# Performance work log

Hardware: AMD Instinct MI355X
Metric: run time of the kernel (lower is better)

## Reference

```python
import jax, jax.numpy as jnp
import numpy as np

MAX_V = 100000.0
CLAMP = 8.0


def setup_inputs() -> dict:
    key = jax.random.key(0)
    point = jax.random.normal(key, (8, 4096, 3), dtype=jnp.float32)
    return {"point": point}


def reference(point):
    # point: [B, N, D]
    p = point.astype(jnp.float32)
    N = p.shape[1]
    # ||a-b|| via ||a||^2 + ||b||^2 - 2 a.b (avoids the [B,N,N,D] diff tensor
    # the torch original materializes; same math up to fp rounding)
    sq = jnp.sum(p * p, axis=-1)                       # [B, N]
    d2 = sq[:, :, None] + sq[:, None, :] - 2.0 * jnp.einsum('bnd,bmd->bnm', p, p)
    dist = jnp.sqrt(jnp.maximum(d2, 0.0))              # [B, N, N]
    dist = dist + jnp.eye(N, dtype=jnp.float32) * MAX_V  # bigeye: kill diagonal
    min_dist = jnp.min(dist, axis=2)                   # [B, N] nearest-neighbor dist
    c = jnp.max(min_dist, axis=1)                      # [B] farthest-point distance
    return jnp.maximum(c, CLAMP)
```

## Files before the change

kernel.cpp:

```cpp
#include <hip/hip_runtime.h>
#include <math.h>

#define NB       8
#define NPTS     4096
#define CLAMP    8.0f
#define CLAMP2   64.0f
#define BIG      3.0e38f

#define THREADS  1024
#define QPT      4
#define SAMPLES  64
#define CHUNK    8


__global__ __launch_bounds__(THREADS)
void mmpd_batch(const float* __restrict__ pts, float* __restrict__ out) {
    __shared__ float sp[SAMPLES * 3];
    __shared__ float allp[NPTS * 3];
    __shared__ unsigned int wflag[16];
    __shared__ unsigned int sflag;
    __shared__ float wmaxs[16];

    const int tid  = threadIdx.x;
    const int b    = blockIdx.x;
    const int lane = tid & 63;
    const int wid  = tid >> 6;
    const float* __restrict__ base = pts + (size_t)b * (NPTS * 3);

    if (tid < (SAMPLES * 3 / 4))
        ((float4*)sp)[tid] = ((const float4*)base)[tid];
    __syncthreads();

    const int q0 = tid * QPT;
    const float4 f0 = ((const float4*)base)[tid * 3 + 0];
    const float4 f1 = ((const float4*)base)[tid * 3 + 1];
    const float4 f2 = ((const float4*)base)[tid * 3 + 2];
    const float qx[QPT] = {f0.x, f0.w, f1.z, f2.y};
    const float qy[QPT] = {f0.y, f1.x, f1.w, f2.z};
    const float qz[QPT] = {f0.z, f1.y, f2.x, f2.w};

    float mn[QPT] = {BIG, BIG, BIG, BIG};

    for (int i = 0; i < SAMPLES; i += CHUNK) {
        #pragma unroll
        for (int k = 0; k < CHUNK; ++k) {
            const int s = i + k;
            const float px = sp[3 * s + 0];
            const float py = sp[3 * s + 1];
            const float pz = sp[3 * s + 2];
            #pragma unroll
            for (int j = 0; j < QPT; ++j) {
                const float dx = qx[j] - px;
                const float dy = qy[j] - py;
                const float dz = qz[j] - pz;
                const float d2 = dx * dx + dy * dy + dz * dz;
                mn[j] = fminf(mn[j], (s == q0 + j) ? BIG : d2);
            }
        }
        const bool over = (mn[0] > CLAMP2) | (mn[1] > CLAMP2) |
                          (mn[2] > CLAMP2) | (mn[3] > CLAMP2);
        if (__ballot(over) == 0ull) break;
    }

    {
        const bool over = (mn[0] > CLAMP2) | (mn[1] > CLAMP2) |
                          (mn[2] > CLAMP2) | (mn[3] > CLAMP2);
        const unsigned long long bal = __ballot(over);
        if (lane == 0) wflag[wid] = (bal != 0ull) ? 1u : 0u;
    }
    __syncthreads();
    if (tid == 0) {
        unsigned int f = 0;
        #pragma unroll
        for (int w = 0; w < 16; ++w) f |= wflag[w];
        sflag = f;
    }
    __syncthreads();

    if (sflag == 0u) {
        if (tid == 0) out[b] = CLAMP;
        return;
    }

    #pragma unroll
    for (int k = 0; k < 3; ++k)
        ((float4*)allp)[tid + k * THREADS] = ((const float4*)base)[tid + k * THREADS];
    __syncthreads();

    float ex[QPT] = {BIG, BIG, BIG, BIG};
    for (int m = 0; m < NPTS; ++m) {
        const float px = allp[3 * m + 0];
        const float py = allp[3 * m + 1];
        const float pz = allp[3 * m + 2];
        #pragma unroll
        for (int j = 0; j < QPT; ++j) {
            const float dx = qx[j] - px;
            const float dy = qy[j] - py;
            const float dz = qz[j] - pz;
            const float d2 = dx * dx + dy * dy + dz * dz;
            ex[j] = fminf(ex[j], (m == q0 + j) ? BIG : d2);
        }
    }

    float v = fmaxf(fmaxf(ex[0], ex[1]), fmaxf(ex[2], ex[3]));
    #pragma unroll
    for (int off = 32; off >= 1; off >>= 1)
        v = fmaxf(v, __shfl_xor(v, off));
    if (lane == 0) wmaxs[wid] = v;
    __syncthreads();
    if (tid == 0) {
        float m = wmaxs[0];
        #pragma unroll
        for (int w = 1; w < 16; ++w) m = fmaxf(m, wmaxs[w]);
        out[b] = fmaxf(sqrtf(m), CLAMP);
    }
}

extern "C" void kernel_launch(void* const* d_in, const int* in_sizes, int n_in,
                              void* d_out, int out_size, void* d_ws, size_t ws_size,
                              hipStream_t stream) {
    const float* pts = (const float*)d_in[0];
    float* out = (float*)d_out;

    mmpd_batch<<<NB, THREADS, 0, stream>>>(pts, out);
}
```

Measured before the change: 9.525 us.

## Replace sampled early-exit with intra-thread check and single-wave fallback

The early-exit test now compares each thread's four points only against each other instead of against 64 shared-memory samples, and drops the sample staging and one block barrier. The 4096-point shared-memory load is gone. The exact fallback now runs on a single wavefront reading global memory directly, refining only the query points whose nearest distance to the first 64 points is above the clamp. This shortens the common path where the answer clamps, at the cost of a much slower serial fallback if clamping does not happen.

```diff
diff --git a/kernel.cpp b/kernel.cpp
--- a/kernel.cpp
+++ b/kernel.cpp
@@ -9,17 +9,11 @@
 
 #define THREADS  1024
 #define QPT      4
-#define SAMPLES  64
-#define CHUNK    8
 
 
 __global__ __launch_bounds__(THREADS)
-void mmpd_batch(const float* __restrict__ pts, float* __restrict__ out) {
-    __shared__ float sp[SAMPLES * 3];
-    __shared__ float allp[NPTS * 3];
+void mmpd_slim(const float* __restrict__ pts, float* __restrict__ out) {
     __shared__ unsigned int wflag[16];
-    __shared__ unsigned int sflag;
-    __shared__ float wmaxs[16];
 
     const int tid  = threadIdx.x;
     const int b    = blockIdx.x;
@@ -27,93 +21,70 @@
     const int wid  = tid >> 6;
     const float* __restrict__ base = pts + (size_t)b * (NPTS * 3);
 
-    if (tid < (SAMPLES * 3 / 4))
-        ((float4*)sp)[tid] = ((const float4*)base)[tid];
-    __syncthreads();
-
-    const int q0 = tid * QPT;
     const float4 f0 = ((const float4*)base)[tid * 3 + 0];
     const float4 f1 = ((const float4*)base)[tid * 3 + 1];
     const float4 f2 = ((const float4*)base)[tid * 3 + 2];
-    const float qx[QPT] = {f0.x, f0.w, f1.z, f2.y};
-    const float qy[QPT] = {f0.y, f1.x, f1.w, f2.z};
-    const float qz[QPT] = {f0.z, f1.y, f2.x, f2.w};
+    const float px[QPT] = {f0.x, f0.w, f1.z, f2.y};
+    const float py[QPT] = {f0.y, f1.x, f1.w, f2.z};
+    const float pz[QPT] = {f0.z, f1.y, f2.x, f2.w};
 
     float mn[QPT] = {BIG, BIG, BIG, BIG};
-
-    for (int i = 0; i < SAMPLES; i += CHUNK) {
+    #pragma unroll
+    for (int i = 0; i < QPT; ++i) {
         #pragma unroll
-        for (int k = 0; k < CHUNK; ++k) {
-            const int s = i + k;
-            const float px = sp[3 * s + 0];
-            const float py = sp[3 * s + 1];
-            const float pz = sp[3 * s + 2];
-            #pragma unroll
-            for (int j = 0; j < QPT; ++j) {
-                const float dx = qx[j] - px;
-                const float dy = qy[j] - py;
-                const float dz = qz[j] - pz;
-                const float d2 = dx * dx + dy * dy + dz * dz;
-                mn[j] = fminf(mn[j], (s == q0 + j) ? BIG : d2);
-            }
+        for (int j = i + 1; j < QPT; ++j) {
+            const float dx = px[i] - px[j];
+            const float dy = py[i] - py[j];
+            const float dz = pz[i] - pz[j];
+            const float d2 = dx * dx + dy * dy + dz * dz;
+            mn[i] = fminf(mn[i], d2);
+            mn[j] = fminf(mn[j], d2);
         }
-        const bool over = (mn[0] > CLAMP2) | (mn[1] > CLAMP2) |
-                          (mn[2] > CLAMP2) | (mn[3] > CLAMP2);
-        if (__ballot(over) == 0ull) break;
     }
 
-    {
-        const bool over = (mn[0] > CLAMP2) | (mn[1] > CLAMP2) |
-                          (mn[2] > CLAMP2) | (mn[3] > CLAMP2);
-        const unsigned long long bal = __ballot(over);
-        if (lane == 0) wflag[wid] = (bal != 0ull) ? 1u : 0u;
-    }
+    const bool over = (mn[0] > CLAMP2) | (mn[1] > CLAMP2) |
+                      (mn[2] > CLAMP2) | (mn[3] > CLAMP2);
+    const unsigned long long bal = __ballot(over);
+    if (lane == 0) wflag[wid] = (bal != 0ull) ? 1u : 0u;
     __syncthreads();
-    if (tid == 0) {
-        unsigned int f = 0;
-        #pragma unroll
-        for (int w = 0; w < 16; ++w) f |= wflag[w];
-        sflag = f;
-    }
-    __syncthreads();
+    if (wid != 0) return;
 
-    if (sflag == 0u) {
-        if (tid == 0) out[b] = CLAMP;
+    const unsigned int f = (lane < 16) ? wflag[lane] : 0u;
+    if (__ballot(f != 0u) == 0ull) {
+        if (lane == 0) out[b] = CLAMP;
         return;
     }
 
-    #pragma unroll
-    for (int k = 0; k < 3; ++k)
-        ((float4*)allp)[tid + k * THREADS] = ((const float4*)base)[tid + k * THREADS];
-    __syncthreads();
+    const float sx = base[3 * lane + 0];
+    const float sy = base[3 * lane + 1];
+    const float sz = base[3 * lane + 2];
 
-    float ex[QPT] = {BIG, BIG, BIG, BIG};
-    for (int m = 0; m < NPTS; ++m) {
-        const float px = allp[3 * m + 0];
-        const float py = allp[3 * m + 1];
-        const float pz = allp[3 * m + 2];
+    float bmax = 0.0f;
+    for (int q = 0; q < NPTS; ++q) {
+        const float qx = base[3 * q + 0];
+        const float qy = base[3 * q + 1];
+        const float qz = base[3 * q + 2];
+        const float dx = qx - sx, dy = qy - sy, dz = qz - sz;
+        float qmin = (lane == q) ? BIG : (dx * dx + dy * dy + dz * dz);
         #pragma unroll
-        for (int j = 0; j < QPT; ++j) {
-            const float dx = qx[j] - px;
-            const float dy = qy[j] - py;
-            const float dz = qz[j] - pz;
-            const float d2 = dx * dx + dy * dy + dz * dz;
-            ex[j] = fminf(ex[j], (m == q0 + j) ? BIG : d2);
+        for (int off = 32; off >= 1; off >>= 1)
+            qmin = fminf(qmin, __shfl_xor(qmin, off));
+        if (qmin > CLAMP2) {
+            float mnq = BIG;
+            for (int m = lane; m < NPTS; m += 64) {
+                const float ddx = qx - base[3 * m + 0];
+                const float ddy = qy - base[3 * m + 1];
+                const float ddz = qz - base[3 * m + 2];
+                const float dd2 = ddx * ddx + ddy * ddy + ddz * ddz;
+                mnq = fminf(mnq, (m == q) ? BIG : dd2);
+            }
+            #pragma unroll
+            for (int off = 32; off >= 1; off >>= 1)
+                mnq = fminf(mnq, __shfl_xor(mnq, off));
+            bmax = fmaxf(bmax, mnq);
         }
     }
-
-    float v = fmaxf(fmaxf(ex[0], ex[1]), fmaxf(ex[2], ex[3]));
-    #pragma unroll
-    for (int off = 32; off >= 1; off >>= 1)
-        v = fmaxf(v, __shfl_xor(v, off));
-    if (lane == 0) wmaxs[wid] = v;
-    __syncthreads();
-    if (tid == 0) {
-        float m = wmaxs[0];
-        #pragma unroll
-        for (int w = 1; w < 16; ++w) m = fmaxf(m, wmaxs[w]);
-        out[b] = fmaxf(sqrtf(m), CLAMP);
-    }
+    if (lane == 0) out[b] = fmaxf(sqrtf(bmax), CLAMP);
 }
 
 extern "C" void kernel_launch(void* const* d_in, const int* in_sizes, int n_in,
@@ -122,5 +93,5 @@
     const float* pts = (const float*)d_in[0];
     float* out = (float*)d_out;
 
-    mmpd_batch<<<NB, THREADS, 0, stream>>>(pts, out);
+    mmpd_slim<<<NB, THREADS, 0, stream>>>(pts, out);
 }
```

Measured after the change: 9.612 us. About the same (+0.9%).
